# Kernel optimization log

Measured on AMD Instinct MI355X. Metric: run time of the kernel, lower is better.

The kernel has to match this reference:

```python
import math
import jax, jax.numpy as jnp
import numpy as np

# gpt-oss config constants (layer_idx=1 -> sliding_window disabled)
HID = 2880
N_HEADS = 64
N_KV = 8
D_HEAD = 64
GROUPS = N_HEADS // N_KV  # 8 query heads per kv head
SLIDING_WINDOW = 0        # layer_idx % 2 == 1 -> full causal attention
SM_SCALE = 1.0 / math.sqrt(D_HEAD)
EPS = 1e-5

ROPE_BASE = 150000.0
INIT_CTX = 4096
SCALING = 32.0
NTK_ALPHA = 1.0
NTK_BETA = 32.0


def _rope_cos_sin(num_tokens: int):
    """YaRN-scaled RoPE tables, fp32, positions 0..num_tokens-1 (offset=0, no cache)."""
    d_half = D_HEAD // 2
    freq = ROPE_BASE ** (np.arange(0, D_HEAD, 2, dtype=np.float64) / D_HEAD)
    concentration = 0.1 * math.log(SCALING) + 1.0
    low = d_half * math.log(INIT_CTX / (NTK_BETA * 2 * math.pi)) / math.log(ROPE_BASE)
    high = d_half * math.log(INIT_CTX / (NTK_ALPHA * 2 * math.pi)) / math.log(ROPE_BASE)
    interpolation = 1.0 / (SCALING * freq)
    extrapolation = 1.0 / freq
    ramp = (np.arange(d_half, dtype=np.float64) - low) / (high - low)
    mask = 1.0 - np.clip(ramp, 0.0, 1.0)
    inv_freq = interpolation * (1.0 - mask) + extrapolation * mask
    t = np.arange(num_tokens, dtype=np.float64)
    freqs = np.outer(t, inv_freq)  # [S, d_half]
    cos = (np.cos(freqs) * concentration).astype(np.float32)
    sin = (np.sin(freqs) * concentration).astype(np.float32)
    return jnp.asarray(cos), jnp.asarray(sin)


def _rotate(x, cos, sin):
    # x: [B, S, nh, D]; cos/sin: [S, D/2]
    c = cos[None, :, None, :]
    s = sin[None, :, None, :]
    x1, x2 = jnp.split(x, 2, axis=-1)
    return jnp.concatenate([x1 * c - x2 * s, x2 * c + x1 * s], axis=-1)


def setup_inputs() -> dict:
    key = jax.random.key(0)
    ks = jax.random.split(key, 5)
    B, S = 1, 1536
    x = jax.random.normal(ks[0], (B, S, HID), dtype=jnp.float32)
    sinks = jax.random.normal(ks[1], (N_HEADS,), dtype=jnp.float32) * 0.5
    norm_scale = jnp.ones((HID,), dtype=jnp.float32)
    qkv_dim = D_HEAD * (N_HEADS + 2 * N_KV)  # 5120
    qkv_w = jax.random.normal(ks[2], (qkv_dim, HID), dtype=jnp.float32) * 0.02
    qkv_b = jnp.zeros((qkv_dim,), dtype=jnp.float32)
    out_w = jax.random.normal(ks[3], (HID, N_HEADS * D_HEAD), dtype=jnp.float32) * 0.02
    out_b = jnp.zeros((HID,), dtype=jnp.float32)
    return {"x": x, "sinks": sinks, "norm_scale": norm_scale,
            "qkv_w": qkv_w, "qkv_b": qkv_b, "out_w": out_w, "out_b": out_b}


def reference(x, sinks, norm_scale, qkv_w, qkv_b, out_w, out_b):
    B, S, _ = x.shape
    # RMSNorm (fp32)
    t = x * jax.lax.rsqrt(jnp.mean(x * x, axis=-1, keepdims=True) + EPS) * norm_scale
    # fused QKV projection
    qkv = jnp.einsum('bsd,od->bso', t, qkv_w) + qkv_b
    q, k, v = jnp.split(qkv, [N_HEADS * D_HEAD, (N_HEADS + N_KV) * D_HEAD], axis=-1)
    q = q.reshape(B, S, N_HEADS, D_HEAD)
    k = k.reshape(B, S, N_KV, D_HEAD)
    v = v.reshape(B, S, N_KV, D_HEAD)
    # RoPE (offset = 0, no cache)
    cos, sin = _rope_cos_sin(S)
    q = _rotate(q, cos, sin)
    k = _rotate(k, cos, sin)
    # GQA: head h = g*N_KV + kv
    q = q.reshape(B, S, GROUPS, N_KV, D_HEAD)
    scores = jnp.einsum('bqgkd,bskd->bgkqs', q, k) * SM_SCALE  # [B,G,KV,S,S]
    i = jnp.arange(S)[:, None]
    j = jnp.arange(S)[None, :]
    allowed = j <= i  # causal
    if SLIDING_WINDOW > 0:
        allowed = allowed & (i - j < SLIDING_WINDOW)
    scores = jnp.where(allowed[None, None, None, :, :], scores, -1e30)
    # softmax with learned per-head sink logit in the denominator
    sink = sinks.reshape(GROUPS, N_KV)[None, :, :, None]  # [1,G,KV,1]
    m = jnp.maximum(jnp.max(scores, axis=-1), sink)       # [B,G,KV,S]
    p = jnp.exp(scores - m[..., None])
    denom = jnp.sum(p, axis=-1) + jnp.exp(sink - m)
    attn = p / denom[..., None]
    o = jnp.einsum('bgkqs,bskd->bqgkd', attn, v).reshape(B, S, N_HEADS * D_HEAD)
    y = jnp.einsum('bse,oe->bso', o, out_w) + out_b
    return x + y
```

## Files before the change

### kernel.cpp

```cpp
#include <hip/hip_runtime.h>
#include <hip/hip_bf16.h>
#include <math.h>

typedef unsigned short u16;
typedef __attribute__((ext_vector_type(8))) short bf16x8;
typedef __attribute__((ext_vector_type(4))) float f32x4;
typedef __attribute__((ext_vector_type(4))) u16 u16x4;
typedef __attribute__((ext_vector_type(8))) u16 u16x8;

#define S_LEN   1536
#define HID     2880
#define NH      64
#define NKV     8
#define DH      64
#define QKV_N   5120
#define QDIM    4096
#define KVDIM   512
#define SMSCALE 0.125f
#define LOG2E   1.44269504f
#define EPSV    1e-5f

__device__ __forceinline__ float b2f(u16 u) {
    unsigned int v = ((unsigned int)u) << 16;
    float f; __builtin_memcpy(&f, &v, 4); return f;
}
__device__ __forceinline__ u16 f2b(float f) {
    __hip_bfloat16 h = __float2bfloat16(f);
    return *reinterpret_cast<u16*>(&h);
}
__device__ __forceinline__ float exp2n(float x) { return __builtin_amdgcn_exp2f(x); }
__device__ __forceinline__ void gld16(const u16* g, u16* l) {
    __builtin_amdgcn_global_load_lds(
        (const __attribute__((address_space(1))) unsigned int*)g,
        (__attribute__((address_space(3))) unsigned int*)l, 16, 0, 0);
}
#define WAIT_VM6()   __builtin_amdgcn_s_waitcnt(0xF76)
#define WAIT_VM4()   __builtin_amdgcn_s_waitcnt(0xF74)
#define WAIT_VM0()   __builtin_amdgcn_s_waitcnt(0xF70)
#define WAIT_LGKM0() __builtin_amdgcn_s_waitcnt(0xC07F)

__device__ __forceinline__ void conv2(const float* __restrict__ src,
                                      u16* __restrict__ dst, int i)
{
    float4 v0 = ((const float4*)src)[2 * i];
    float4 v1 = ((const float4*)src)[2 * i + 1];
    u16x8 o;
    o[0] = f2b(v0.x); o[1] = f2b(v0.y); o[2] = f2b(v0.z); o[3] = f2b(v0.w);
    o[4] = f2b(v1.x); o[5] = f2b(v1.y); o[6] = f2b(v1.z); o[7] = f2b(v1.w);
    ((u16x8*)dst)[i] = o;
}

__global__ __launch_bounds__(256) void prep_kernel(
    const float* __restrict__ qkv_w, u16* __restrict__ qkv_w_bf,
    const float* __restrict__ x, const float* __restrict__ ns, u16* __restrict__ t,
    float* __restrict__ cosT, float* __restrict__ sinT,
    const float* __restrict__ out_w, u16* __restrict__ out_w_bf)
{
    __shared__ float red[4];
    const int b = blockIdx.x;
    const int tid = threadIdx.x;
    if (b < 7200) {
        conv2(qkv_w, qkv_w_bf, b * 256 + tid);
    } else if (b < 8736) {
        const int s = b - 7200;
        const float4* xr4 = (const float4*)(x + (size_t)s * HID);
        float ss = 0.f;
        for (int i = tid; i < 720; i += 256) {
            float4 v = xr4[i];
            ss += v.x * v.x + v.y * v.y + v.z * v.z + v.w * v.w;
        }
        for (int off = 32; off > 0; off >>= 1) ss += __shfl_down(ss, off);
        if ((tid & 63) == 0) red[tid >> 6] = ss;
        __syncthreads();
        float tot = red[0] + red[1] + red[2] + red[3];
        float scale = rsqrtf(tot / (float)HID + EPSV);
        const float4* ns4 = (const float4*)ns;
        u16x4* tr4 = (u16x4*)(t + (size_t)s * HID);
        for (int i = tid; i < 720; i += 256) {
            float4 v = xr4[i];
            float4 nv = ns4[i];
            u16x4 o;
            o.x = f2b(v.x * scale * nv.x);
            o.y = f2b(v.y * scale * nv.y);
            o.z = f2b(v.z * scale * nv.z);
            o.w = f2b(v.w * scale * nv.w);
            tr4[i] = o;
        }
    } else if (b < 8928) {
        int idx = (b - 8736) * 256 + tid;
        if (idx >= S_LEN * 32) return;
        int s = idx >> 5, i = idx & 31;
        const double PI2 = 6.283185307179586476925286766559;
        double base = 150000.0;
        double freq = pow(base, (double)(2 * i) / 64.0);
        double conc = 0.1 * log(32.0) + 1.0;
        double low  = 32.0 * log(4096.0 / (32.0 * PI2)) / log(base);
        double high = 32.0 * log(4096.0 / (1.0  * PI2)) / log(base);
        double interp = 1.0 / (32.0 * freq);
        double extrap = 1.0 / freq;
        double ramp = ((double)i - low) / (high - low);
        double msk = 1.0 - fmin(fmax(ramp, 0.0), 1.0);
        double invf = interp * (1.0 - msk) + extrap * msk;
        double ang = (double)s * invf;
        cosT[idx] = (float)(cos(ang) * conc);
        sinT[idx] = (float)(sin(ang) * conc);
    } else {
        conv2(out_w, out_w_bf, (b - 8928) * 256 + tid);
    }
}

__global__ __launch_bounds__(256) void conv_bf16_kernel(
    const float* __restrict__ src, u16* __restrict__ dst)
{
    conv2(src, dst, blockIdx.x * 256 + threadIdx.x);
}

__global__ __launch_bounds__(512, 2) void gemm_bt_8p_kernel(
    const u16* __restrict__ A, const u16* __restrict__ B,
    u16* __restrict__ Cp, u16* __restrict__ Cp2, u16* __restrict__ Cp3,
    int M, int N, int K, int it0, int it1, int ntm, int ntn)
{
    extern __shared__ __align__(16) u16 smem[];
    u16* sAp = smem;
    u16* sBp = smem + 32768;

    const int tid  = threadIdx.x;
    const int wave = tid >> 6, lane = tid & 63;
    const int quad = lane >> 4, l16 = lane & 15;
    const int wm = wave >> 2, wn = wave & 3;

    const int nwg  = gridDim.x;
    const int q8   = nwg >> 3, r8 = nwg & 7;
    const int flat = blockIdx.x;
    const int xcd  = flat & 7, loc = flat >> 3;
    const int swz  = (xcd < r8) ? xcd * (q8 + 1) + loc
                                : r8 * (q8 + 1) + (xcd - r8) * q8 + loc;
    const int tpz  = ntm * ntn;
    const int z    = swz / tpz;
    const int rem  = swz - z * tpz;
    const int nt   = rem / ntm;
    const int mt   = rem - nt * ntm;
    const int bm = mt * 256, bn = nt * 256;
    const int niter = z ? it1 : it0;
    const int kb    = z ? (it0 + (z - 1) * it1) * 64 : 0;
    u16* C = (z == 0) ? Cp : (z == 1) ? (Cp + (size_t)M * N) : (z == 2) ? Cp2 : Cp3;

    const int r2  = tid >> 2;
    const int ks8 = (tid & 3) * 8;
    const u16* gA0 = A + (size_t)(bm + r2) * K + kb + ks8;
    const u16* gA1 = gA0 + (size_t)128 * K;
    int brA = bn + r2;       if (brA > N - 1) brA = N - 1;
    int brB = bn + 128 + r2; if (brB > N - 1) brB = N - 1;
    const u16* gB0 = B + (size_t)brA * K + kb + ks8;
    const u16* gB1 = B + (size_t)brB * K + kb + ks8;
    const int sw = wave * 512;

    f32x4 acc[8][4];
    #pragma unroll
    for (int i = 0; i < 8; i++)
        #pragma unroll
        for (int j = 0; j < 4; j++) acc[i][j] = (f32x4){0.f, 0.f, 0.f, 0.f};

    auto stA = [&](int c, int kh, int t) {
        u16* d = sAp + (((c << 1) | kh) << 13);
        const int koff = t * 64 + kh * 32;
        gld16(gA0 + koff, d + sw);
        gld16(gA1 + koff, d + 4096 + sw);
    };
    auto stB = [&](int c, int kh, int t) {
        u16* d = sBp + (((c << 1) | kh) << 13);
        const int koff = t * 64 + kh * 32;
        gld16(gB0 + koff, d + sw);
        gld16(gB1 + koff, d + 4096 + sw);
    };

    bf16x8 bv[4];
    const int arow = wm * 128 + l16;
    const int brow = wn * 64 + l16;
    auto rdB = [&](int c, int ks) {
        const u16* p = sBp + (((c << 1) | ks) << 13) + brow * 32 + quad * 8;
        #pragma unroll
        for (int nf = 0; nf < 4; nf++) bv[nf] = *(const bf16x8*)(p + nf * 16 * 32);
    };
    auto mmph = [&](int c, int ks, int mh) {
        const u16* p = sAp + (((c << 1) | ks) << 13) + (arow + mh * 64) * 32 + quad * 8;
        bf16x8 av[4];
        #pragma unroll
        for (int mf = 0; mf < 4; mf++) av[mf] = *(const bf16x8*)(p + mf * 16 * 32);
        __builtin_amdgcn_s_setprio(1);
        #pragma unroll
        for (int mf = 0; mf < 4; mf++)
            #pragma unroll
            for (int nf = 0; nf < 4; nf++)
                acc[mh * 4 + mf][nf] = __builtin_amdgcn_mfma_f32_16x16x32_bf16(
                    av[mf], bv[nf], acc[mh * 4 + mf][nf], 0, 0, 0);
        __builtin_amdgcn_s_setprio(0);
    };

    stA(0, 0, 0); stB(0, 0, 0); stA(0, 1, 0); stB(0, 1, 0);

    for (int t = 0; t < niter - 1; ++t) {
        const int c = t & 1;
        stA(c ^ 1, 0, t + 1);
        WAIT_VM6();
        __builtin_amdgcn_s_barrier();
        rdB(c, 0); mmph(c, 0, 0);
        stB(c ^ 1, 0, t + 1);
        mmph(c, 0, 1);
        stA(c ^ 1, 1, t + 1);
        WAIT_VM6();
        __builtin_amdgcn_s_barrier();
        rdB(c, 1); mmph(c, 1, 0);
        stB(c ^ 1, 1, t + 1);
        mmph(c, 1, 1);
    }
    {
        const int c = (niter - 1) & 1;
        WAIT_VM4();
        __builtin_amdgcn_s_barrier();
        rdB(c, 0); mmph(c, 0, 0); mmph(c, 0, 1);
        WAIT_VM0();
        __builtin_amdgcn_s_barrier();
        rdB(c, 1); mmph(c, 1, 0); mmph(c, 1, 1);
    }

    #pragma unroll
    for (int im = 0; im < 8; im++) {
        const int row0 = bm + wm * 128 + im * 16 + quad * 4;
        #pragma unroll
        for (int nf = 0; nf < 4; nf++) {
            const int col = bn + wn * 64 + nf * 16 + l16;
            if (col < N) {
                #pragma unroll
                for (int r = 0; r < 4; r++)
                    C[(size_t)(row0 + r) * N + col] = f2b(acc[im][nf][r]);
            }
        }
    }
}

__global__ __launch_bounds__(256) void rope_apply_kernel(
    const u16* __restrict__ p0, const u16* __restrict__ p1, const float* __restrict__ bias,
    const float* __restrict__ cosT, const float* __restrict__ sinT,
    u16* __restrict__ q_r, u16* __restrict__ k_r, u16* __restrict__ vt)
{
    __shared__ u16 tile[64][72];
    const int b = blockIdx.x;
    const int tid = threadIdx.x;
    if (b < 1728) {
        int idx = b * 256 + tid;
        int s = idx / 288;
        int c = idx - s * 288;
        const u16* r0p = p0 + (size_t)s * QKV_N;
        const u16* r1p = p1 + (size_t)s * QKV_N;
        int hh = c >> 2, j0 = (c & 3) * 8;
        int off = hh * 64;
        u16x8 a1 = *(const u16x8*)(r0p + off + j0);
        u16x8 b1 = *(const u16x8*)(r1p + off + j0);
        u16x8 a2 = *(const u16x8*)(r0p + off + 32 + j0);
        u16x8 b2 = *(const u16x8*)(r1p + off + 32 + j0);
        float bl[8], bh[8], cc[8], sn[8];
        *(float4*)&bl[0] = *(const float4*)(bias + off + j0);
        *(float4*)&bl[4] = *(const float4*)(bias + off + j0 + 4);
        *(float4*)&bh[0] = *(const float4*)(bias + off + 32 + j0);
        *(float4*)&bh[4] = *(const float4*)(bias + off + 32 + j0 + 4);
        *(float4*)&cc[0] = *(const float4*)(cosT + s * 32 + j0);
        *(float4*)&cc[4] = *(const float4*)(cosT + s * 32 + j0 + 4);
        *(float4*)&sn[0] = *(const float4*)(sinT + s * 32 + j0);
        *(float4*)&sn[4] = *(const float4*)(sinT + s * 32 + j0 + 4);
        const float scale = (hh < 64) ? SMSCALE * LOG2E : 1.0f;
        u16x8 lo, hi;
        #pragma unroll
        for (int j = 0; j < 8; j++) {
            float x1 = b2f(a1[j]) + b2f(b1[j]) + bl[j];
            float x2 = b2f(a2[j]) + b2f(b2[j]) + bh[j];
            lo[j] = f2b((x1 * cc[j] - x2 * sn[j]) * scale);
            hi[j] = f2b((x2 * cc[j] + x1 * sn[j]) * scale);
        }
        if (hh < 64) {
            u16* dst = q_r + (size_t)s * QDIM + off;
            *(u16x8*)(dst + j0) = lo;
            *(u16x8*)(dst + 32 + j0) = hi;
        } else {
            u16* dst = k_r + (size_t)s * KVDIM + (hh - 64) * 64;
            *(u16x8*)(dst + j0) = lo;
            *(u16x8*)(dst + 32 + j0) = hi;
        }
    } else {
        int vb = b - 1728;
        int kvh = vb / 24, sblk = vb - kvh * 24;
        int s0 = sblk * 64;
        int r = tid >> 3;
        int cc = (tid & 7) * 8;
        int off = QDIM + KVDIM + kvh * 64 + cc;
        float bb[8];
        *(float4*)&bb[0] = *(const float4*)(bias + off);
        *(float4*)&bb[4] = *(const float4*)(bias + off + 4);
        #pragma unroll
        for (int rr = 0; rr < 64; rr += 32) {
            int s = s0 + r + rr;
            u16x8 a = *(const u16x8*)(p0 + (size_t)s * QKV_N + off);
            u16x8 b2 = *(const u16x8*)(p1 + (size_t)s * QKV_N + off);
            #pragma unroll
            for (int j = 0; j < 8; j++)
                tile[cc + j][r + rr] = f2b(b2f(a[j]) + b2f(b2[j]) + bb[j]);
        }
        __syncthreads();
        #pragma unroll
        for (int rr = 0; rr < 64; rr += 32) {
            uint4 ov;
            u16* p = (u16*)&ov;
            #pragma unroll
            for (int j = 0; j < 8; j++) p[j] = tile[r + rr][cc + j];
            *(uint4*)(vt + (size_t)(kvh * 64 + r + rr) * S_LEN + s0 + cc) = ov;
        }
    }
}

__global__ __launch_bounds__(256) void attn_kernel(
    const u16* __restrict__ q_r, const u16* __restrict__ k_r, const u16* __restrict__ vt,
    const float* __restrict__ sinks, u16* __restrict__ o)
{
    __shared__ __align__(16) u16 sK[2][64 * 72];
    __shared__ __align__(16) u16 sVt[2][64 * 72];
    __shared__ __align__(16) u16 sP[4 * 16 * 72];

    const int bx = blockIdx.x, h = blockIdx.y;
    const int kvh = h & 7;
    const int tid = threadIdx.x, wave = tid >> 6, lane = tid & 63;
    const int quad = lane >> 4, l16 = lane & 15;
    const int srow = tid >> 3;
    const int scol = (tid & 7) * 8;
    u16* sPw = sP + wave * 16 * 72;
    const float sinkv = sinks[h] * LOG2E;

    bf16x8 vone;
    #pragma unroll
    for (int j = 0; j < 8; j++) vone[j] = (short)0x3F80;

    uint4 kreg0, kreg1, vreg0, vreg1;
    const u16* kbase = k_r + (size_t)srow * KVDIM + kvh * 64 + scol;
    const u16* vbase = vt + (size_t)(kvh * 64 + srow) * S_LEN + scol;

    auto issue = [&](int j0) {
        kreg0 = *(const uint4*)(kbase + (size_t)j0 * KVDIM);
        kreg1 = *(const uint4*)(kbase + (size_t)(j0 + 32) * KVDIM);
        vreg0 = *(const uint4*)(vbase + j0);
        vreg1 = *(const uint4*)(vbase + (size_t)32 * S_LEN + j0);
    };
    auto lwrite = [&](int c) {
        *(uint4*)(&sK[c][srow * 72 + scol])        = kreg0;
        *(uint4*)(&sK[c][(srow + 32) * 72 + scol]) = kreg1;
        *(uint4*)(&sVt[c][srow * 72 + scol])        = vreg0;
        *(uint4*)(&sVt[c][(srow + 32) * 72 + scol]) = vreg1;
    };

    for (int phase = 0; phase < 2; ++phase) {
        const int qt = phase ? (23 - bx) : bx;
        const int q_i = qt * 64 + wave * 16 + l16;
        const u16* qp = q_r + (size_t)q_i * QDIM + h * 64 + quad * 8;
        bf16x8 aq0 = *(const bf16x8*)(qp);
        bf16x8 aq1 = *(const bf16x8*)(qp + 32);

        float m_i = sinkv, l_i = 1.0f;
        f32x4 acc[4];
        #pragma unroll
        for (int dt = 0; dt < 4; dt++) acc[dt] = (f32x4){0.f, 0.f, 0.f, 0.f};

        const int ntile = qt + 1;
        issue(0);
        __syncthreads();

        for (int tt = 0; tt < ntile; ++tt) {
            const int c = tt & 1;
            lwrite(c);
            if (tt + 1 < ntile) issue((tt + 1) * 64);
            WAIT_LGKM0();
            __builtin_amdgcn_s_barrier();

            f32x4 sc[4];
            __builtin_amdgcn_s_setprio(1);
            #pragma unroll
            for (int nt = 0; nt < 4; nt++) {
                const u16* kp = &sK[c][(nt * 16 + l16) * 72 + quad * 8];
                bf16x8 bk0 = *(const bf16x8*)(kp);
                bf16x8 bk1 = *(const bf16x8*)(kp + 32);
                f32x4 s0 = (f32x4){0.f, 0.f, 0.f, 0.f};
                s0 = __builtin_amdgcn_mfma_f32_16x16x32_bf16(bk0, aq0, s0, 0, 0, 0);
                s0 = __builtin_amdgcn_mfma_f32_16x16x32_bf16(bk1, aq1, s0, 0, 0, 0);
                sc[nt] = s0;
            }
            __builtin_amdgcn_s_setprio(0);

            if (tt == qt) {
                #pragma unroll
                for (int nt = 0; nt < 4; nt++)
                    #pragma unroll
                    for (int r = 0; r < 4; r++)
                        if (tt * 64 + nt * 16 + quad * 4 + r > q_i) sc[nt][r] = -INFINITY;
            }

            float a0 = fmaxf(fmaxf(sc[0][0], sc[0][1]), sc[0][2]);
            float a1 = fmaxf(fmaxf(sc[0][3], sc[1][0]), sc[1][1]);
            float a2 = fmaxf(fmaxf(sc[1][2], sc[1][3]), sc[2][0]);
            float a3 = fmaxf(fmaxf(sc[2][1], sc[2][2]), sc[2][3]);
            float a4 = fmaxf(fmaxf(sc[3][0], sc[3][1]), sc[3][2]);
            float vmax = fmaxf(fmaxf(fmaxf(a0, a1), fmaxf(a2, a3)),
                               fmaxf(a4, sc[3][3]));
            vmax = fmaxf(vmax, __shfl_xor(vmax, 16));
            vmax = fmaxf(vmax, __shfl_xor(vmax, 32));
            if (__any(vmax > m_i + 11.0f)) {
                float mnew = fmaxf(m_i, vmax);
                float alpha = exp2n(m_i - mnew);
                l_i *= alpha;
                #pragma unroll
                for (int dt = 0; dt < 4; dt++)
                    #pragma unroll
                    for (int r = 0; r < 4; r++) acc[dt][r] *= alpha;
                m_i = mnew;
            }
            u16x4 pk[4];
            #pragma unroll
            for (int nt = 0; nt < 4; nt++) {
                #pragma unroll
                for (int r = 0; r < 4; r++)
                    pk[nt][r] = f2b(exp2n(sc[nt][r] - m_i));
            }
            #pragma unroll
            for (int nt = 0; nt < 4; nt++)
                *(u16x4*)(sPw + l16 * 72 + nt * 16 + quad * 4) = pk[nt];
            __threadfence_block();

            bf16x8 ap0 = *(const bf16x8*)(sPw + l16 * 72 + quad * 8);
            bf16x8 ap1 = *(const bf16x8*)(sPw + l16 * 72 + 32 + quad * 8);
            __builtin_amdgcn_s_setprio(1);
            f32x4 lsum = (f32x4){0.f, 0.f, 0.f, 0.f};
            lsum = __builtin_amdgcn_mfma_f32_16x16x32_bf16(vone, ap0, lsum, 0, 0, 0);
            lsum = __builtin_amdgcn_mfma_f32_16x16x32_bf16(vone, ap1, lsum, 0, 0, 0);
            #pragma unroll
            for (int dt = 0; dt < 4; dt++) {
                const u16* vp = &sVt[c][(dt * 16 + l16) * 72 + quad * 8];
                bf16x8 bv0 = *(const bf16x8*)(vp);
                bf16x8 bv1 = *(const bf16x8*)(vp + 32);
                acc[dt] = __builtin_amdgcn_mfma_f32_16x16x32_bf16(bv0, ap0, acc[dt], 0, 0, 0);
                acc[dt] = __builtin_amdgcn_mfma_f32_16x16x32_bf16(bv1, ap1, acc[dt], 0, 0, 0);
            }
            __builtin_amdgcn_s_setprio(0);
            l_i += lsum[0];
        }

        float inv = 1.0f / l_i;
        #pragma unroll
        for (int dt = 0; dt < 4; dt++) {
            u16x4 ov;
            #pragma unroll
            for (int r = 0; r < 4; r++) ov[r] = f2b(acc[dt][r] * inv);
            *(u16x4*)(o + (size_t)q_i * QDIM + h * 64 + dt * 16 + quad * 4) = ov;
        }
    }
}

__global__ __launch_bounds__(256) void final_add_kernel(
    const u16* __restrict__ p0, const u16* __restrict__ p1, const u16* __restrict__ p2,
    const u16* __restrict__ p3, int np,
    const float* __restrict__ bias, const float* __restrict__ x, float* __restrict__ out)
{
    int i = blockIdx.x * 256 + threadIdx.x;
    int base = i * 8;
    int col = base % HID;
    float4 xo0 = *(const float4*)(x + base);
    float4 xo1 = *(const float4*)(x + base + 4);
    float4 bi0 = *(const float4*)(bias + col);
    float4 bi1 = *(const float4*)(bias + col + 4);
    u16x8 a = ((const u16x8*)p0)[i];
    u16x8 b = ((const u16x8*)p1)[i];
    u16x8 c = ((const u16x8*)p2)[i];
    float s[8];
    #pragma unroll
    for (int j = 0; j < 8; j++) s[j] = b2f(a[j]) + b2f(b[j]) + b2f(c[j]);
    if (np == 4) {
        u16x8 d = ((const u16x8*)p3)[i];
        #pragma unroll
        for (int j = 0; j < 8; j++) s[j] += b2f(d[j]);
    }
    float4 r0, r1;
    r0.x = s[0] + bi0.x + xo0.x;
    r0.y = s[1] + bi0.y + xo0.y;
    r0.z = s[2] + bi0.z + xo0.z;
    r0.w = s[3] + bi0.w + xo0.w;
    r1.x = s[4] + bi1.x + xo1.x;
    r1.y = s[5] + bi1.y + xo1.y;
    r1.z = s[6] + bi1.z + xo1.z;
    r1.w = s[7] + bi1.w + xo1.w;
    *(float4*)(out + base) = r0;
    *(float4*)(out + base + 4) = r1;
}

extern "C" void kernel_launch(void* const* d_in, const int* in_sizes, int n_in,
                              void* d_out, int out_size, void* d_ws, size_t ws_size,
                              hipStream_t stream)
{
    const float* x          = (const float*)d_in[0];
    const float* sinks      = (const float*)d_in[1];
    const float* norm_scale = (const float*)d_in[2];
    const float* qkv_w      = (const float*)d_in[3];
    const float* qkv_b      = (const float*)d_in[4];
    const float* out_w      = (const float*)d_in[5];
    const float* out_b      = (const float*)d_in[6];
    float* out = (float*)d_out;

    char* ws = (char*)d_ws;
    u16* t        = (u16*)(ws);
    u16* qkv_w_bf = (u16*)(ws + 8847360);
    u16* qkvp0    = (u16*)(ws + 38338560);
    u16* qkvp1    = (u16*)(ws + 54067200);
    float* cosT   = (float*)(ws + 69795840);
    float* sinT   = (float*)(ws + 69992448);
    u16* k_r      = (u16*)(ws);
    u16* vt       = (u16*)(ws + 1572864);
    u16* q_r      = (u16*)(ws + 3145728);
    u16* o        = (u16*)(ws + 15728640);
    u16* outp0    = (u16*)(ws + 28311552);
    u16* outp1    = (u16*)(ws + 37158912);
    u16* outp2    = (u16*)(ws + 3145728);

    const bool fuse_outw = (ws_size >= 93782016ull);
    u16* out_w_bf = fuse_outw ? (u16*)(ws + 70189056) : (u16*)(ws + 46006272);

    static bool lds_attr_set = false;
    if (!lds_attr_set) {
        hipFuncSetAttribute(reinterpret_cast<const void*>(gemm_bt_8p_kernel),
                            hipFuncAttributeMaxDynamicSharedMemorySize, 131072);
        lds_attr_set = true;
    }

    prep_kernel<<<fuse_outw ? 14688 : 8928, 256, 0, stream>>>(
        qkv_w, qkv_w_bf, x, norm_scale, t, cosT, sinT, out_w, out_w_bf);
    gemm_bt_8p_kernel<<<240, 512, 131072, stream>>>(
        t, qkv_w_bf, qkvp0, qkvp0, qkvp0, S_LEN, QKV_N, HID, 23, 22, 6, 20);
    rope_apply_kernel<<<1920, 256, 0, stream>>>(
        qkvp0, qkvp1, qkv_b, cosT, sinT, q_r, k_r, vt);
    if (!fuse_outw)
        conv_bf16_kernel<<<5760, 256, 0, stream>>>(out_w, out_w_bf);
    attn_kernel<<<dim3(12, NH), 256, 0, stream>>>(q_r, k_r, vt, sinks, o);
    gemm_bt_8p_kernel<<<216, 512, 131072, stream>>>(
        o, out_w_bf, outp0, outp2, outp2, S_LEN, HID, QDIM, 22, 21, 6, 12);
    final_add_kernel<<<S_LEN * HID / 8 / 256, 256, 0, stream>>>(
        outp0, outp1, outp2, outp2, 3, out_b, x, out);
}
```

Measured before the change: 306.9 us.

## Fuse fp32-to-bf16 weight conversion into GEMM B-tile loading

Removes the separate passes that converted the qkv and out weights to bf16. Each GEMM now loads fp32 B tiles into registers, converts them, and writes them to LDS, with the next tile's global load issued after the barrier. This cuts a full read and write of the weight matrices plus a kernel launch. The cost is twice the global bytes for B inside the GEMM, extra VGPR pressure, and LDS-write/lgkm waits on the GEMM critical path.

```diff
diff --git a/kernel.cpp b/kernel.cpp
--- a/kernel.cpp
+++ b/kernel.cpp
@@ -35,34 +35,18 @@
         (__attribute__((address_space(3))) unsigned int*)l, 16, 0, 0);
 }
 #define WAIT_VM6()   __builtin_amdgcn_s_waitcnt(0xF76)
-#define WAIT_VM4()   __builtin_amdgcn_s_waitcnt(0xF74)
 #define WAIT_VM0()   __builtin_amdgcn_s_waitcnt(0xF70)
 #define WAIT_LGKM0() __builtin_amdgcn_s_waitcnt(0xC07F)
 
-__device__ __forceinline__ void conv2(const float* __restrict__ src,
-                                      u16* __restrict__ dst, int i)
-{
-    float4 v0 = ((const float4*)src)[2 * i];
-    float4 v1 = ((const float4*)src)[2 * i + 1];
-    u16x8 o;
-    o[0] = f2b(v0.x); o[1] = f2b(v0.y); o[2] = f2b(v0.z); o[3] = f2b(v0.w);
-    o[4] = f2b(v1.x); o[5] = f2b(v1.y); o[6] = f2b(v1.z); o[7] = f2b(v1.w);
-    ((u16x8*)dst)[i] = o;
-}
-
 __global__ __launch_bounds__(256) void prep_kernel(
-    const float* __restrict__ qkv_w, u16* __restrict__ qkv_w_bf,
     const float* __restrict__ x, const float* __restrict__ ns, u16* __restrict__ t,
-    float* __restrict__ cosT, float* __restrict__ sinT,
-    const float* __restrict__ out_w, u16* __restrict__ out_w_bf)
+    float* __restrict__ cosT, float* __restrict__ sinT)
 {
     __shared__ float red[4];
     const int b = blockIdx.x;
     const int tid = threadIdx.x;
-    if (b < 7200) {
-        conv2(qkv_w, qkv_w_bf, b * 256 + tid);
-    } else if (b < 8736) {
-        const int s = b - 7200;
+    if (b < 1536) {
+        const int s = b;
         const float4* xr4 = (const float4*)(x + (size_t)s * HID);
         float ss = 0.f;
         for (int i = tid; i < 720; i += 256) {
@@ -86,8 +70,8 @@
             o.w = f2b(v.w * scale * nv.w);
             tr4[i] = o;
         }
-    } else if (b < 8928) {
-        int idx = (b - 8736) * 256 + tid;
+    } else {
+        int idx = (b - 1536) * 256 + tid;
         if (idx >= S_LEN * 32) return;
         int s = idx >> 5, i = idx & 31;
         const double PI2 = 6.283185307179586476925286766559;
@@ -104,19 +88,11 @@
         double ang = (double)s * invf;
         cosT[idx] = (float)(cos(ang) * conc);
         sinT[idx] = (float)(sin(ang) * conc);
-    } else {
-        conv2(out_w, out_w_bf, (b - 8928) * 256 + tid);
-    }
-}
-
-__global__ __launch_bounds__(256) void conv_bf16_kernel(
-    const float* __restrict__ src, u16* __restrict__ dst)
-{
-    conv2(src, dst, blockIdx.x * 256 + threadIdx.x);
+    }
 }
 
 __global__ __launch_bounds__(512, 2) void gemm_bt_8p_kernel(
-    const u16* __restrict__ A, const u16* __restrict__ B,
+    const u16* __restrict__ A, const float* __restrict__ B,
     u16* __restrict__ Cp, u16* __restrict__ Cp2, u16* __restrict__ Cp3,
     int M, int N, int K, int it0, int it1, int ntm, int ntn)
 {
@@ -151,8 +127,8 @@
     const u16* gA1 = gA0 + (size_t)128 * K;
     int brA = bn + r2;       if (brA > N - 1) brA = N - 1;
     int brB = bn + 128 + r2; if (brB > N - 1) brB = N - 1;
-    const u16* gB0 = B + (size_t)brA * K + kb + ks8;
-    const u16* gB1 = B + (size_t)brB * K + kb + ks8;
+    const float* gB0 = B + (size_t)brA * K + kb + ks8;
+    const float* gB1 = B + (size_t)brB * K + kb + ks8;
     const int sw = wave * 512;
 
     f32x4 acc[8][4];
@@ -167,11 +143,30 @@
         gld16(gA0 + koff, d + sw);
         gld16(gA1 + koff, d + 4096 + sw);
     };
-    auto stB = [&](int c, int kh, int t) {
-        u16* d = sBp + (((c << 1) | kh) << 13);
-        const int koff = t * 64 + kh * 32;
-        gld16(gB0 + koff, d + sw);
-        gld16(gB1 + koff, d + 4096 + sw);
+
+    float4 p0a, p0b, p0c, p0d;
+    float4 p1a, p1b, p1c, p1d;
+    auto bissue0 = [&](int t) {
+        const float* q0 = gB0 + t * 64;
+        const float* q1 = gB1 + t * 64;
+        p0a = *(const float4*)q0; p0b = *(const float4*)(q0 + 4);
+        p0c = *(const float4*)q1; p0d = *(const float4*)(q1 + 4);
+    };
+    auto bissue1 = [&](int t) {
+        const float* q0 = gB0 + t * 64 + 32;
+        const float* q1 = gB1 + t * 64 + 32;
+        p1a = *(const float4*)q0; p1b = *(const float4*)(q0 + 4);
+        p1c = *(const float4*)q1; p1d = *(const float4*)(q1 + 4);
+    };
+    auto bwr = [&](int c, int kh, float4 va, float4 vb, float4 vc, float4 vd) {
+        u16* d = sBp + (((c << 1) | kh) << 13) + tid * 8;
+        bf16x8 o0, o1;
+        o0[0] = f2b(va.x); o0[1] = f2b(va.y); o0[2] = f2b(va.z); o0[3] = f2b(va.w);
+        o0[4] = f2b(vb.x); o0[5] = f2b(vb.y); o0[6] = f2b(vb.z); o0[7] = f2b(vb.w);
+        o1[0] = f2b(vc.x); o1[1] = f2b(vc.y); o1[2] = f2b(vc.z); o1[3] = f2b(vc.w);
+        o1[4] = f2b(vd.x); o1[5] = f2b(vd.y); o1[6] = f2b(vd.z); o1[7] = f2b(vd.w);
+        *(bf16x8*)d = o0;
+        *(bf16x8*)(d + 4096) = o1;
     };
 
     bf16x8 bv[4];
@@ -197,29 +192,37 @@
         __builtin_amdgcn_s_setprio(0);
     };
 
-    stA(0, 0, 0); stB(0, 0, 0); stA(0, 1, 0); stB(0, 1, 0);
+    stA(0, 0, 0); stA(0, 1, 0);
+    bissue0(0); bissue1(0);
 
     for (int t = 0; t < niter - 1; ++t) {
         const int c = t & 1;
         stA(c ^ 1, 0, t + 1);
+        bwr(c, 0, p0a, p0b, p0c, p0d);
         WAIT_VM6();
+        WAIT_LGKM0();
         __builtin_amdgcn_s_barrier();
+        bissue0(t + 1);
         rdB(c, 0); mmph(c, 0, 0);
-        stB(c ^ 1, 0, t + 1);
         mmph(c, 0, 1);
         stA(c ^ 1, 1, t + 1);
+        bwr(c, 1, p1a, p1b, p1c, p1d);
         WAIT_VM6();
+        WAIT_LGKM0();
         __builtin_amdgcn_s_barrier();
+        bissue1(t + 1);
         rdB(c, 1); mmph(c, 1, 0);
-        stB(c ^ 1, 1, t + 1);
         mmph(c, 1, 1);
     }
     {
         const int c = (niter - 1) & 1;
-        WAIT_VM4();
+        bwr(c, 0, p0a, p0b, p0c, p0d);
+        WAIT_VM0();
+        WAIT_LGKM0();
         __builtin_amdgcn_s_barrier();
         rdB(c, 0); mmph(c, 0, 0); mmph(c, 0, 1);
-        WAIT_VM0();
+        bwr(c, 1, p1a, p1b, p1c, p1d);
+        WAIT_LGKM0();
         __builtin_amdgcn_s_barrier();
         rdB(c, 1); mmph(c, 1, 0); mmph(c, 1, 1);
     }
@@ -462,7 +465,6 @@
 
 __global__ __launch_bounds__(256) void final_add_kernel(
     const u16* __restrict__ p0, const u16* __restrict__ p1, const u16* __restrict__ p2,
-    const u16* __restrict__ p3, int np,
     const float* __restrict__ bias, const float* __restrict__ x, float* __restrict__ out)
 {
     int i = blockIdx.x * 256 + threadIdx.x;
@@ -478,11 +480,6 @@
     float s[8];
     #pragma unroll
     for (int j = 0; j < 8; j++) s[j] = b2f(a[j]) + b2f(b[j]) + b2f(c[j]);
-    if (np == 4) {
-        u16x8 d = ((const u16x8*)p3)[i];
-        #pragma unroll
-        for (int j = 0; j < 8; j++) s[j] += b2f(d[j]);
-    }
     float4 r0, r1;
     r0.x = s[0] + bi0.x + xo0.x;
     r0.y = s[1] + bi0.y + xo0.y;
@@ -511,7 +508,6 @@
 
     char* ws = (char*)d_ws;
     u16* t        = (u16*)(ws);
-    u16* qkv_w_bf = (u16*)(ws + 8847360);
     u16* qkvp0    = (u16*)(ws + 38338560);
     u16* qkvp1    = (u16*)(ws + 54067200);
     float* cosT   = (float*)(ws + 69795840);
@@ -524,9 +520,6 @@
     u16* outp1    = (u16*)(ws + 37158912);
     u16* outp2    = (u16*)(ws + 3145728);
 
-    const bool fuse_outw = (ws_size >= 93782016ull);
-    u16* out_w_bf = fuse_outw ? (u16*)(ws + 70189056) : (u16*)(ws + 46006272);
-
     static bool lds_attr_set = false;
     if (!lds_attr_set) {
         hipFuncSetAttribute(reinterpret_cast<const void*>(gemm_bt_8p_kernel),
@@ -534,17 +527,14 @@
         lds_attr_set = true;
     }
 
-    prep_kernel<<<fuse_outw ? 14688 : 8928, 256, 0, stream>>>(
-        qkv_w, qkv_w_bf, x, norm_scale, t, cosT, sinT, out_w, out_w_bf);
+    prep_kernel<<<1728, 256, 0, stream>>>(x, norm_scale, t, cosT, sinT);
     gemm_bt_8p_kernel<<<240, 512, 131072, stream>>>(
-        t, qkv_w_bf, qkvp0, qkvp0, qkvp0, S_LEN, QKV_N, HID, 23, 22, 6, 20);
+        t, qkv_w, qkvp0, qkvp0, qkvp0, S_LEN, QKV_N, HID, 23, 22, 6, 20);
     rope_apply_kernel<<<1920, 256, 0, stream>>>(
         qkvp0, qkvp1, qkv_b, cosT, sinT, q_r, k_r, vt);
-    if (!fuse_outw)
-        conv_bf16_kernel<<<5760, 256, 0, stream>>>(out_w, out_w_bf);
     attn_kernel<<<dim3(12, NH), 256, 0, stream>>>(q_r, k_r, vt, sinks, o);
     gemm_bt_8p_kernel<<<216, 512, 131072, stream>>>(
-        o, out_w_bf, outp0, outp2, outp2, S_LEN, HID, QDIM, 22, 21, 6, 12);
+        o, out_w, outp0, outp2, outp2, S_LEN, HID, QDIM, 22, 21, 6, 12);
     final_add_kernel<<<S_LEN * HID / 8 / 256, 256, 0, stream>>>(
-        outp0, outp1, outp2, outp2, 3, out_b, x, out);
-}
+        outp0, outp1, outp2, out_b, x, out);
+}
```

Measured after the change: 310.0 us. No clear change (+1.0%).
